# Performance work log

Hardware: AMD Instinct MI355X
Metric: run time of the kernel (lower is better)

The kernel has to match this reference:

```python
import jax, jax.numpy as jnp
import numpy as np

D_MODEL = 2048
N_HEADS = 16
D_KEY = D_MODEL // N_HEADS
ALIBI_SLOPE = 8.0
KEY_SCALE = D_KEY ** -0.5
B, S = 2, 2048


def setup_inputs() -> dict:
    key = jax.random.key(0)
    ks = jax.random.split(key, 12)
    sd = D_MODEL ** -0.5
    return {
        "states": jax.random.normal(ks[0], (B, S, D_MODEL), jnp.float32),
        "bias_mask": jax.random.normal(ks[1], (B, S, S), jnp.float32),
        # weights stored [in, out] (torch Linear applies x @ W.T + b)
        "wq": jax.random.normal(ks[2], (D_MODEL, D_MODEL), jnp.float32) * sd,
        "bq": jnp.zeros((D_MODEL,), jnp.float32),
        "wk": jax.random.normal(ks[3], (D_MODEL, D_MODEL), jnp.float32) * sd,
        "bk": jnp.zeros((D_MODEL,), jnp.float32),
        "wv": jax.random.normal(ks[4], (D_MODEL, D_MODEL), jnp.float32) * sd,
        "bv": jnp.zeros((D_MODEL,), jnp.float32),
        "wg": jax.random.normal(ks[5], (D_MODEL, N_HEADS), jnp.float32) * sd,
        "bg": jnp.zeros((N_HEADS,), jnp.float32),
        "wo": jax.random.normal(ks[6], (D_MODEL, D_MODEL), jnp.float32) * sd,
        "bo": jnp.zeros((D_MODEL,), jnp.float32),
    }


def reference(states, bias_mask, wq, bq, wk, bk, wv, bv, wg, bg, wo, bo):
    # head_scale = exp2(-(h+1)*alibi_slope/n_heads), non-trainable buffer
    head_scale = jnp.exp2(-(jnp.arange(N_HEADS, dtype=jnp.float32) + 1.0)
                          * ALIBI_SLOPE / N_HEADS)
    # [B, H, Q, K] bias with per-head ALiBi scaling
    bias = bias_mask[:, None, :, :] * head_scale[None, :, None, None]

    def heads(x, w, b):  # [B,S,D] -> [B,H,S,Dk]
        y = x @ w + b
        return y.reshape(x.shape[0], x.shape[1], N_HEADS, D_KEY).transpose(0, 2, 1, 3)

    q = heads(states, wq, bq)
    k = heads(states, wk, bk)
    v = heads(states, wv, bv)

    scores = jnp.einsum('bhqd,bhkd->bhqk', q, k) * KEY_SCALE + bias
    probs = jax.nn.softmax(scores, axis=-1)
    o = jnp.einsum('bhqk,bhkd->bqhd', probs, v)  # [B,S,H,Dk]

    g = jax.nn.sigmoid(states @ wg + bg)  # [B,S,H] head gate
    o = o * g[..., None]

    return o.reshape(o.shape[0], o.shape[1], D_MODEL) @ wo + bo
```

## Files before the change

### kernel.cpp

```cpp
#include <hip/hip_runtime.h>
#include <hip/hip_bf16.h>

#define SEQ 2048
#define DM 2048
#define NH 16
#define DK 128
#define LOG2E 1.4426950408889634f
#define QK_SCALE 0.08838834764831845f

typedef __attribute__((ext_vector_type(8))) short short8;
typedef __attribute__((ext_vector_type(4))) float f32x4;
typedef __attribute__((ext_vector_type(4))) unsigned short us4;

__device__ __forceinline__ unsigned short f2b(float f) {
  union { float f; unsigned u; } v; v.f = f;
  unsigned r = v.u + 0x7fffu + ((v.u >> 16) & 1u);
  return (unsigned short)(r >> 16);
}
__device__ __forceinline__ float b2f(unsigned short v) {
  union { unsigned u; float f; } x; x.u = ((unsigned)v) << 16; return x.f;
}

__device__ __forceinline__ void gl_lds16(const void* g, void* l) {
  __builtin_amdgcn_global_load_lds((const __attribute__((address_space(1))) void*)g,
                                   (__attribute__((address_space(3))) void*)l, 16, 0, 0);
}

#define SBAR()   __builtin_amdgcn_s_barrier()
#define SCHED0() __builtin_amdgcn_sched_barrier(0)
#define LGKM0()  asm volatile("s_waitcnt lgkmcnt(0)" ::: "memory")

__global__ __launch_bounds__(256) void cast_bf16_kernel(const float* __restrict__ in,
                                                        unsigned short* __restrict__ out) {
  int i = blockIdx.x * 256 + threadIdx.x;
  const float4* p = (const float4*)in;
  float4 a = p[2*i], b = p[2*i+1];
  us4 r0, r1;
  r0[0]=f2b(a.x); r0[1]=f2b(a.y); r0[2]=f2b(a.z); r0[3]=f2b(a.w);
  r1[0]=f2b(b.x); r1[1]=f2b(b.y); r1[2]=f2b(b.z); r1[3]=f2b(b.w);
  us4* o = (us4*)out;
  o[2*i] = r0; o[2*i+1] = r1;
}

__global__ __launch_bounds__(256) void transpose_cast_kernel(const float* __restrict__ w,
                                                             unsigned short* __restrict__ wt) {
  __shared__ float t[64][65];
  int c0 = blockIdx.x * 64, r0 = blockIdx.y * 64;
  int tid = threadIdx.x;
  int rr = tid >> 4;
  int c4 = (tid & 15) * 4;
#pragma unroll
  for (int p = 0; p < 4; ++p) {
    int r = p*16 + rr;
    float4 v = *(const float4*)&w[(size_t)(r0 + r)*DM + c0 + c4];
    t[r][c4] = v.x; t[r][c4+1] = v.y; t[r][c4+2] = v.z; t[r][c4+3] = v.w;
  }
  __syncthreads();
#pragma unroll
  for (int p = 0; p < 4; ++p) {
    int c = p*16 + rr;
    us4 v;
    v[0] = f2b(t[c4+0][c]); v[1] = f2b(t[c4+1][c]);
    v[2] = f2b(t[c4+2][c]); v[3] = f2b(t[c4+3][c]);
    *(us4*)&wt[(size_t)(c0 + c)*DM + r0 + c4] = v;
  }
}

__global__ __launch_bounds__(256) void transpose_wg_kernel(const float* __restrict__ wg,
                                                           unsigned short* __restrict__ wgT) {
  int idx = blockIdx.x * 256 + threadIdx.x;
  int c = idx & 15;
  int r0 = (idx >> 4) * 4;
#pragma unroll
  for (int r = 0; r < 4; ++r)
    wgT[(size_t)c*DM + r0 + r] = f2b(wg[(size_t)(r0 + r)*NH + c]);
}

__device__ __forceinline__ void gemm256_core(const unsigned short* __restrict__ A,
                                             const unsigned short* __restrict__ Bt,
                                             int m0, int n0, f32x4 (&acc)[8][4]) {
  __shared__ __align__(16) unsigned short Ab[2][2][8192];
  __shared__ __align__(16) unsigned short Bb[2][2][8192];
  const int TK = DM / 64;

  int tid = threadIdx.x, wid = tid >> 6, lane = tid & 63;
  int lo = lane & 15, hi = lane >> 4;
  int wm = wid >> 2, wn = wid & 3;
  int w2 = wid * 2;

  int srow8 = lane >> 3;
  int skb = (((lane & 7) ^ srow8) << 4);
  const char* Ag = (const char*)A;
  const char* Bg = (const char*)Bt;

#define STG_A(S,CUR) do {                                                          \
    const char* g = Ag + (size_t)(S)*128 + skb;                                    \
    char* l = (char*)&Ab[CUR][0][0] + w2*1024;                                     \
    gl_lds16(g + (size_t)(m0 + w2*8 + srow8)*4096,           l);                   \
    gl_lds16(g + (size_t)(m0 + w2*8 + 8 + srow8)*4096,       l + 1024);            \
    gl_lds16(g + (size_t)(m0 + 128 + w2*8 + srow8)*4096,     l + 16384);           \
    gl_lds16(g + (size_t)(m0 + 128 + w2*8 + 8 + srow8)*4096, l + 16384 + 1024);    \
  } while(0)
#define STG_B(S,CUR) do {                                                          \
    const char* g = Bg + (size_t)(S)*128 + skb;                                    \
    char* l = (char*)&Bb[CUR][0][0] + w2*1024;                                     \
    gl_lds16(g + (size_t)(n0 + w2*8 + srow8)*4096,           l);                   \
    gl_lds16(g + (size_t)(n0 + w2*8 + 8 + srow8)*4096,       l + 1024);            \
    gl_lds16(g + (size_t)(n0 + 128 + w2*8 + srow8)*4096,     l + 16384);           \
    gl_lds16(g + (size_t)(n0 + 128 + w2*8 + 8 + srow8)*4096, l + 16384 + 1024);    \
  } while(0)

#pragma unroll
  for (int i = 0; i < 8; ++i)
#pragma unroll
    for (int j = 0; j < 4; ++j) acc[i][j] = (f32x4){0.f,0.f,0.f,0.f};

  STG_B(0,0); STG_A(0,0); STG_B(1,1); STG_A(1,1);
  asm volatile("s_waitcnt vmcnt(8)" ::: "memory");
  SBAR();

  int msk = (lo & 7) << 4;
  int k0 = (hi*16) ^ msk;
  int k1 = (64 + hi*16) ^ msk;
  int brow = (wn & 1) * 64;

  short8 a[4][2], bA[2][2], bB[2][2];

#define MF16(MH,NH,BF)                                                              \
  __builtin_amdgcn_s_setprio(1);                                                    \
  _Pragma("unroll") for (int mm = 0; mm < 4; ++mm)                                  \
  _Pragma("unroll") for (int nn = 0; nn < 2; ++nn) {                                \
    acc[(MH)*4+mm][(NH)*2+nn] = __builtin_amdgcn_mfma_f32_16x16x32_bf16(            \
        a[mm][0], BF[nn][0], acc[(MH)*4+mm][(NH)*2+nn], 0, 0, 0);                   \
    acc[(MH)*4+mm][(NH)*2+nn] = __builtin_amdgcn_mfma_f32_16x16x32_bf16(            \
        a[mm][1], BF[nn][1], acc[(MH)*4+mm][(NH)*2+nn], 0, 0, 0);                   \
  }                                                                                 \
  __builtin_amdgcn_s_setprio(0);

  for (int s = 0; s < TK; ++s) {
    int cur = s & 1;
    const char* Ac = (const char*)&Ab[cur][wm][0];
    const char* Bc = (const char*)&Bb[cur][wn >> 1][0];
    bool pre = (s + 2) < TK;

#pragma unroll
    for (int mm = 0; mm < 4; ++mm) {
      a[mm][0] = *(const short8*)(Ac + (mm*16 + lo)*128 + k0);
      a[mm][1] = *(const short8*)(Ac + (mm*16 + lo)*128 + k1);
    }
#pragma unroll
    for (int nn = 0; nn < 2; ++nn) {
      bA[nn][0] = *(const short8*)(Bc + (brow + nn*16 + lo)*128 + k0);
      bA[nn][1] = *(const short8*)(Bc + (brow + nn*16 + lo)*128 + k1);
    }
    SBAR(); LGKM0(); SCHED0();
    MF16(0, 0, bA);
    SBAR();

#pragma unroll
    for (int nn = 0; nn < 2; ++nn) {
      bB[nn][0] = *(const short8*)(Bc + (brow + (2+nn)*16 + lo)*128 + k0);
      bB[nn][1] = *(const short8*)(Bc + (brow + (2+nn)*16 + lo)*128 + k1);
    }
    SBAR(); LGKM0(); SCHED0();
    MF16(0, 1, bB);
    SBAR();

#pragma unroll
    for (int mm = 0; mm < 4; ++mm) {
      a[mm][0] = *(const short8*)(Ac + ((64 + mm*16 + lo)*128) + k0);
      a[mm][1] = *(const short8*)(Ac + ((64 + mm*16 + lo)*128) + k1);
    }
    if (pre) STG_B(s + 2, cur);
    SBAR(); LGKM0(); SCHED0();
    MF16(1, 0, bA);
    SBAR();

    if (pre) {
      STG_A(s + 2, cur);
      asm volatile("s_waitcnt vmcnt(8)" ::: "memory");
    } else if (s == TK - 2) {
      asm volatile("s_waitcnt vmcnt(0)" ::: "memory");
    }
    SBAR();
    MF16(1, 1, bB);
    SBAR();
  }
#undef STG_A
#undef STG_B
#undef MF16
}

__global__ __launch_bounds__(512, 2) void gemm256_qkv_kernel(const unsigned short* __restrict__ A,
                                                             const unsigned short* __restrict__ Bt,
                                                             const float* __restrict__ bq,
                                                             const float* __restrict__ bk,
                                                             const float* __restrict__ bv,
                                                             unsigned short* __restrict__ QB,
                                                             unsigned short* __restrict__ KB,
                                                             unsigned short* __restrict__ VTB) {
  f32x4 acc[8][4];
  int n0 = blockIdx.x * 256, m0 = blockIdx.y * 256;
  gemm256_core(A, Bt, m0, n0, acc);

  int tid = threadIdx.x, wid = tid >> 6, lane = tid & 63;
  int lo = lane & 15, hi = lane >> 4;
  int wm = wid >> 2, wn = wid & 3;
  int sect = n0 >> 11;

  if (sect == 2) {
#pragma unroll
    for (int mi = 0; mi < 8; ++mi) {
      int m = m0 + wm*128 + mi*16 + 4*hi;
      int b = m >> 11, srow = m & 2047;
#pragma unroll
      for (int nf = 0; nf < 4; ++nf) {
        int n = n0 + wn*64 + nf*16 + lo;
        int nl = n & 2047, h = nl >> 7, d = nl & 127;
        float bvv = bv[nl];
        us4 pk;
#pragma unroll
        for (int r = 0; r < 4; ++r) pk[r] = f2b(acc[mi][nf][r] + bvv);
        *(us4*)&VTB[(((size_t)(b*NH + h))*DK + d)*SEQ + srow] = pk;
      }
    }
  } else {
    unsigned short* out = sect ? KB : QB;
    const float* bp = sect ? bk : bq;
    const float qs = sect ? 1.f : QK_SCALE * LOG2E;
#pragma unroll
    for (int mi = 0; mi < 8; ++mi) {
#pragma unroll
      for (int nf = 0; nf < 4; ++nf) {
        int n = n0 + wn*64 + nf*16 + lo;
        int nl = n & 2047, h = nl >> 7, d = nl & 127;
        float bvv = bp[nl];
#pragma unroll
        for (int r = 0; r < 4; ++r) {
          int m = m0 + wm*128 + mi*16 + 4*hi + r;
          int b = m >> 11, srow = m & 2047;
          out[(((size_t)(b*NH + h))*SEQ + srow)*DK + d] = f2b((acc[mi][nf][r] + bvv) * qs);
        }
      }
    }
  }
}

__global__ __launch_bounds__(512, 2) void gemm256_ao_kernel(const unsigned short* __restrict__ A,
                                                            const unsigned short* __restrict__ Bt,
                                                            const float* __restrict__ bias,
                                                            float* __restrict__ out) {
  f32x4 acc[8][4];
  int n0 = blockIdx.x * 256, m0 = blockIdx.y * 256;
  gemm256_core(A, Bt, m0, n0, acc);

  int tid = threadIdx.x, wid = tid >> 6, lane = tid & 63;
  int lo = lane & 15, hi = lane >> 4;
  int wm = wid >> 2, wn = wid & 3;
#pragma unroll
  for (int mi = 0; mi < 8; ++mi) {
#pragma unroll
    for (int nf = 0; nf < 4; ++nf) {
      int n = n0 + wn*64 + nf*16 + lo;
      float bvv = bias[n];
#pragma unroll
      for (int r = 0; r < 4; ++r) {
        int m = m0 + wm*128 + mi*16 + 4*hi + r;
        out[(size_t)m*DM + n] = acc[mi][nf][r] + bvv;
      }
    }
  }
}

__global__ __launch_bounds__(256) void gate_mfma_kernel(const unsigned short* __restrict__ XB,
                                                        const unsigned short* __restrict__ wgT,
                                                        const float* __restrict__ bg,
                                                        float* __restrict__ G) {
  int tid = threadIdx.x, wid = tid >> 6, lane = tid & 63;
  int lo = lane & 15, hi = lane >> 4;
  int m0 = blockIdx.x * 64 + wid * 16;

  f32x4 acc = {0.f, 0.f, 0.f, 0.f};
  const unsigned short* xrow = XB + (size_t)(m0 + lo) * DM + hi * 8;
  const unsigned short* grow = wgT + (size_t)lo * DM + hi * 8;
#pragma unroll 4
  for (int kt = 0; kt < DM; kt += 32) {
    short8 a = *(const short8*)(xrow + kt);
    short8 b = *(const short8*)(grow + kt);
    acc = __builtin_amdgcn_mfma_f32_16x16x32_bf16(a, b, acc, 0, 0, 0);
  }
  float bgv = bg[lo];
#pragma unroll
  for (int r = 0; r < 4; ++r) {
    float x = acc[r] + bgv;
    G[(size_t)(m0 + 4*hi + r) * NH + lo] = 1.f / (1.f + __builtin_amdgcn_exp2f(-x * LOG2E));
  }
}

__global__ __attribute__((amdgpu_flat_work_group_size(512,512)))
__attribute__((amdgpu_waves_per_eu(2,4)))
void attn_kernel(const unsigned short* __restrict__ Q,
                 const unsigned short* __restrict__ Kb,
                 const unsigned short* __restrict__ VT,
                 const unsigned short* __restrict__ biasb,
                 const float* __restrict__ G,
                 unsigned short* __restrict__ OG) {
  __shared__ __align__(16) unsigned short kbuf[2][64*128];
  __shared__ __align__(16) unsigned short vbuf[2][128*64];
  __shared__ __align__(16) unsigned short pbuf[8*16*64];

  int bid = blockIdx.x;
  int h  = bid & 15;
  int b  = (bid >> 4) & 1;
  int qt = bid >> 5;
  int bh = b*NH + h;

  int tid = threadIdx.x, wid = tid >> 6, lane = tid & 63;
  int lo = lane & 15, hi = lane >> 4;
  int qw0 = qt*128 + wid*16;

  float hs2 = __builtin_amdgcn_exp2f(-(float)(h+1) * 0.5f) * LOG2E;

  short8 qf[4];
#pragma unroll
  for (int ks = 0; ks < 4; ++ks)
    qf[ks] = *(const short8*)&Q[((size_t)bh*SEQ + qw0 + lo)*DK + ks*32 + hi*8];

  f32x4 zero4 = {0.f,0.f,0.f,0.f};
  f32x4 acco[8];
#pragma unroll
  for (int f = 0; f < 8; ++f) acco[f] = zero4;
  float lrun[4];
#pragma unroll
  for (int r = 0; r < 4; ++r) lrun[r] = 0.f;

  const char* kbase = (const char*)Kb + ((size_t)bh*SEQ)*DK*2;
  const char* vbase = (const char*)VT + ((size_t)bh*DK)*SEQ*2;
  const unsigned short* bb = biasb + ((size_t)b*SEQ + qw0 + 4*hi)*SEQ + lo;
  char* pb = (char*)pbuf + wid*2048;

  int s16 = lane >> 4, srow8 = lane >> 3;
  int kof = (lane & 15) * 16, vof = (lane & 7) * 16;
  int w2 = wid * 2;

#define STAGE_KV(KT, BUF) do {                                                        \
    _Pragma("unroll")                                                                 \
    for (int c = 0; c < 2; ++c) {                                                     \
      int krc = (w2 + c)*4 + s16;                                                     \
      gl_lds16(kbase + (size_t)((KT) + krc)*256 + (kof ^ ((krc & 7) << 4)),           \
               (char*)kbuf[BUF] + (w2 + c)*1024);                                     \
      int vrc = (w2 + c)*8 + srow8;                                                   \
      gl_lds16(vbase + (size_t)vrc*4096 + (size_t)(KT)*2 + (vof ^ (srow8 << 4)),      \
               (char*)vbuf[BUF] + (w2 + c)*1024);                                     \
    }                                                                                 \
  } while(0)

  unsigned short br[4][4];
#pragma unroll
  for (int r = 0; r < 4; ++r)
#pragma unroll
    for (int nf = 0; nf < 4; ++nf)
      br[r][nf] = bb[(size_t)r*SEQ + nf*16];
  STAGE_KV(0, 0);
  STAGE_KV(64, 1);
  asm volatile("s_waitcnt vmcnt(4)" ::: "memory");
  SBAR();

  const int NT = SEQ / 64;
  int cur = 0;
  for (int t = 0; t < NT; ++t) {
    f32x4 sf[4];
    __builtin_amdgcn_s_setprio(1);
#pragma unroll
    for (int nf = 0; nf < 4; ++nf) {
      f32x4 a = zero4;
#pragma unroll
      for (int ks = 0; ks < 4; ++ks) {
        int krw = nf*16 + lo;
        int cb = (ks*32 + hi*8)*2;
        short8 kf = *(const short8*)((const char*)kbuf[cur] + krw*256 + (cb ^ ((krw & 7) << 4)));
        a = __builtin_amdgcn_mfma_f32_16x16x32_bf16(qf[ks], kf, a, 0, 0, 0);
      }
      sf[nf] = a;
    }
    __builtin_amdgcn_s_setprio(0);

#pragma unroll
    for (int r = 0; r < 4; ++r) {
      int prow = 4*hi + r;
#pragma unroll
      for (int nf = 0; nf < 4; ++nf) {
        float s = fmaf(b2f(br[r][nf]), hs2, sf[nf][r]);
        float p = __builtin_amdgcn_exp2f(s);
        lrun[r] += p;
        *(unsigned short*)(pb + prow*128 + ((((nf*16 + lo)*2)) ^ ((prow & 7) << 4))) = f2b(p);
      }
    }

    short8 pf[2];
#pragma unroll
    for (int ks = 0; ks < 2; ++ks)
      pf[ks] = *(const short8*)(pb + lo*128 + ((ks*64 + hi*16) ^ ((lo & 7) << 4)));
    __builtin_amdgcn_s_setprio(1);
#pragma unroll
    for (int f = 0; f < 8; ++f) {
#pragma unroll
      for (int ks = 0; ks < 2; ++ks) {
        int vrw = f*16 + lo;
        int cb = (ks*32 + hi*8)*2;
        short8 vf = *(const short8*)((const char*)vbuf[cur] + vrw*128 + (cb ^ ((vrw & 7) << 4)));
        acco[f] = __builtin_amdgcn_mfma_f32_16x16x32_bf16(pf[ks], vf, acco[f], 0, 0, 0);
      }
    }
    __builtin_amdgcn_s_setprio(0);

    LGKM0(); SBAR();

    bool more1 = (t + 1) < NT;
    bool more2 = (t + 2) < NT;
    if (more1) {
      int ktn = (t + 1) * 64;
#pragma unroll
      for (int r = 0; r < 4; ++r)
#pragma unroll
        for (int nf = 0; nf < 4; ++nf)
          br[r][nf] = bb[(size_t)r*SEQ + ktn + nf*16];
    }
    if (more2) {
      STAGE_KV((t + 2) * 64, cur);
      asm volatile("s_waitcnt vmcnt(20)" ::: "memory");
    } else if (more1) {
      asm volatile("s_waitcnt vmcnt(16)" ::: "memory");
    }
    SBAR();
    cur ^= 1;
  }
#undef STAGE_KV

#pragma unroll
  for (int r = 0; r < 4; ++r) {
    float l = lrun[r];
    l += __shfl_xor(l, 1); l += __shfl_xor(l, 2);
    l += __shfl_xor(l, 4); l += __shfl_xor(l, 8);
    lrun[r] = l;
  }

#pragma unroll
  for (int r = 0; r < 4; ++r) {
    int qrow = qw0 + 4*hi + r;
    float inv = 1.f / lrun[r];
    float g = G[((size_t)(b*SEQ + qrow))*NH + h];
    float sgl = inv * g;
#pragma unroll
    for (int f = 0; f < 8; ++f)
      OG[((size_t)(b*SEQ) + qrow)*DM + h*DK + f*16 + lo] = f2b(acco[f][r] * sgl);
  }
}

extern "C" void kernel_launch(void* const* d_in, const int* in_sizes, int n_in,
                              void* d_out, int out_size, void* d_ws, size_t ws_size,
                              hipStream_t stream) {
  const float* states    = (const float*)d_in[0];
  const float* bias_mask = (const float*)d_in[1];
  const float* wq = (const float*)d_in[2];
  const float* bq = (const float*)d_in[3];
  const float* wk = (const float*)d_in[4];
  const float* bk = (const float*)d_in[5];
  const float* wv = (const float*)d_in[6];
  const float* bv = (const float*)d_in[7];
  const float* wg = (const float*)d_in[8];
  const float* bg = (const float*)d_in[9];
  const float* wo = (const float*)d_in[10];
  const float* bo = (const float*)d_in[11];

  char* ws = (char*)d_ws;
  unsigned short* XB   = (unsigned short*)(ws + 0);
  unsigned short* OGB  = XB;
  unsigned short* WQVT = (unsigned short*)(ws + 16777216UL);
  unsigned short* WQT  = WQVT;
  unsigned short* WKT  = (unsigned short*)(ws + 25165824UL);
  unsigned short* WVT  = (unsigned short*)(ws + 33554432UL);
  unsigned short* WOT  = (unsigned short*)(ws + 41943040UL);
  unsigned short* QB   = (unsigned short*)(ws + 50331648UL);
  unsigned short* KB   = (unsigned short*)(ws + 67108864UL);
  unsigned short* VTB  = (unsigned short*)(ws + 83886080UL);
  unsigned short* BIASB= (unsigned short*)(ws + 100663296UL);
  float*          GB   = (float*)         (ws + 117440512UL);
  unsigned short* WGT  = (unsigned short*)(ws + 117702656UL);

  cast_bf16_kernel<<<4096, 256, 0, stream>>>(states, XB);
  cast_bf16_kernel<<<4096, 256, 0, stream>>>(bias_mask, BIASB);
  dim3 tg(32, 32);
  transpose_cast_kernel<<<tg, 256, 0, stream>>>(wq, WQT);
  transpose_cast_kernel<<<tg, 256, 0, stream>>>(wk, WKT);
  transpose_cast_kernel<<<tg, 256, 0, stream>>>(wv, WVT);
  transpose_cast_kernel<<<tg, 256, 0, stream>>>(wo, WOT);
  transpose_wg_kernel<<<32, 256, 0, stream>>>(wg, WGT);

  gemm256_qkv_kernel<<<dim3(24, 16), 512, 0, stream>>>(XB, WQVT, bq, bk, bv, QB, KB, VTB);

  gate_mfma_kernel<<<64, 256, 0, stream>>>(XB, WGT, bg, GB);

  attn_kernel<<<512, 512, 0, stream>>>(QB, KB, VTB, BIASB, GB, OGB);

  gemm256_ao_kernel<<<dim3(8, 16), 512, 0, stream>>>(OGB, WOT, bo, (float*)d_out);
}
```

Measured before the change: 375.1 us.

## Read fp32 bias directly in attention, batch weight transposes, reuse K buffer for P

Drops the separate bias-to-bf16 cast kernel; the attention kernel now loads the fp32 bias mask directly, which adds bias bytes read there but removes a full write and re-read pass. Merges the four weight transpose-cast launches into one 3D-grid launch. Removes the dedicated P LDS buffer and writes probabilities into the current K buffer after an extra barrier. This lowers LDS use, possibly raising occupancy, at the cost of an extra sync per tile.

```diff
diff --git a/kernel.cpp b/kernel.cpp
--- a/kernel.cpp
+++ b/kernel.cpp
@@ -42,8 +42,13 @@
   o[2*i] = r0; o[2*i+1] = r1;
 }
 
-__global__ __launch_bounds__(256) void transpose_cast_kernel(const float* __restrict__ w,
-                                                             unsigned short* __restrict__ wt) {
+__global__ __launch_bounds__(256) void transpose_cast4_kernel(const float* __restrict__ w0,
+                                                              const float* __restrict__ w1,
+                                                              const float* __restrict__ w2,
+                                                              const float* __restrict__ w3,
+                                                              unsigned short* __restrict__ dst) {
+  const float* w = (blockIdx.z == 0) ? w0 : (blockIdx.z == 1) ? w1 : (blockIdx.z == 2) ? w2 : w3;
+  unsigned short* wt = dst + (size_t)blockIdx.z * DM * DM;
   __shared__ float t[64][65];
   int c0 = blockIdx.x * 64, r0 = blockIdx.y * 64;
   int tid = threadIdx.x;
@@ -302,12 +307,11 @@
 void attn_kernel(const unsigned short* __restrict__ Q,
                  const unsigned short* __restrict__ Kb,
                  const unsigned short* __restrict__ VT,
-                 const unsigned short* __restrict__ biasb,
+                 const float* __restrict__ biasb,
                  const float* __restrict__ G,
                  unsigned short* __restrict__ OG) {
   __shared__ __align__(16) unsigned short kbuf[2][64*128];
   __shared__ __align__(16) unsigned short vbuf[2][128*64];
-  __shared__ __align__(16) unsigned short pbuf[8*16*64];
 
   int bid = blockIdx.x;
   int h  = bid & 15;
@@ -336,8 +340,7 @@
 
   const char* kbase = (const char*)Kb + ((size_t)bh*SEQ)*DK*2;
   const char* vbase = (const char*)VT + ((size_t)bh*DK)*SEQ*2;
-  const unsigned short* bb = biasb + ((size_t)b*SEQ + qw0 + 4*hi)*SEQ + lo;
-  char* pb = (char*)pbuf + wid*2048;
+  const float* bb = biasb + ((size_t)b*SEQ + qw0 + 4*hi)*SEQ + lo;
 
   int s16 = lane >> 4, srow8 = lane >> 3;
   int kof = (lane & 15) * 16, vof = (lane & 7) * 16;
@@ -355,7 +358,7 @@
     }                                                                                 \
   } while(0)
 
-  unsigned short br[4][4];
+  float br[4][4];
 #pragma unroll
   for (int r = 0; r < 4; ++r)
 #pragma unroll
@@ -385,12 +388,15 @@
     }
     __builtin_amdgcn_s_setprio(0);
 
+    LGKM0(); SBAR();
+    char* pb = (char*)kbuf[cur] + wid*2048;
+
 #pragma unroll
     for (int r = 0; r < 4; ++r) {
       int prow = 4*hi + r;
 #pragma unroll
       for (int nf = 0; nf < 4; ++nf) {
-        float s = fmaf(b2f(br[r][nf]), hs2, sf[nf][r]);
+        float s = fmaf(br[r][nf], hs2, sf[nf][r]);
         float p = __builtin_amdgcn_exp2f(s);
         lrun[r] += p;
         *(unsigned short*)(pb + prow*128 + ((((nf*16 + lo)*2)) ^ ((prow & 7) << 4))) = f2b(p);
@@ -477,31 +483,22 @@
   unsigned short* XB   = (unsigned short*)(ws + 0);
   unsigned short* OGB  = XB;
   unsigned short* WQVT = (unsigned short*)(ws + 16777216UL);
-  unsigned short* WQT  = WQVT;
-  unsigned short* WKT  = (unsigned short*)(ws + 25165824UL);
-  unsigned short* WVT  = (unsigned short*)(ws + 33554432UL);
   unsigned short* WOT  = (unsigned short*)(ws + 41943040UL);
   unsigned short* QB   = (unsigned short*)(ws + 50331648UL);
   unsigned short* KB   = (unsigned short*)(ws + 67108864UL);
   unsigned short* VTB  = (unsigned short*)(ws + 83886080UL);
-  unsigned short* BIASB= (unsigned short*)(ws + 100663296UL);
   float*          GB   = (float*)         (ws + 117440512UL);
   unsigned short* WGT  = (unsigned short*)(ws + 117702656UL);
 
   cast_bf16_kernel<<<4096, 256, 0, stream>>>(states, XB);
-  cast_bf16_kernel<<<4096, 256, 0, stream>>>(bias_mask, BIASB);
-  dim3 tg(32, 32);
-  transpose_cast_kernel<<<tg, 256, 0, stream>>>(wq, WQT);
-  transpose_cast_kernel<<<tg, 256, 0, stream>>>(wk, WKT);
-  transpose_cast_kernel<<<tg, 256, 0, stream>>>(wv, WVT);
-  transpose_cast_kernel<<<tg, 256, 0, stream>>>(wo, WOT);
+  transpose_cast4_kernel<<<dim3(32, 32, 4), 256, 0, stream>>>(wq, wk, wv, wo, WQVT);
   transpose_wg_kernel<<<32, 256, 0, stream>>>(wg, WGT);
 
   gemm256_qkv_kernel<<<dim3(24, 16), 512, 0, stream>>>(XB, WQVT, bq, bk, bv, QB, KB, VTB);
 
   gate_mfma_kernel<<<64, 256, 0, stream>>>(XB, WGT, bg, GB);
 
-  attn_kernel<<<512, 512, 0, stream>>>(QB, KB, VTB, BIASB, GB, OGB);
+  attn_kernel<<<512, 512, 0, stream>>>(QB, KB, VTB, bias_mask, GB, OGB);
 
   gemm256_ao_kernel<<<dim3(8, 16), 512, 0, stream>>>(OGB, WOT, bo, (float*)d_out);
 }
```

New measurement: 368.4 us. No clear change (-1.8%).
